# Optimization experiments

Hardware: AMD Instinct MI355X
Metric: run time of the kernel (lower is better)

## Reference

```python
import jax, jax.numpy as jnp
import numpy as np

NA = 100000   # author nodes
NP = 100000   # paper nodes
E = 500000    # edges per relation
H = 128       # hidden size
FA = 256      # author input features
FP = 128      # paper input features
LA = 4        # author labels
LP = 7        # paper labels


def setup_inputs() -> dict:
    key = jax.random.key(0)
    ks = iter(jax.random.split(key, 48))
    def rn(shape, scale=0.05):
        return jax.random.normal(next(ks), shape, jnp.float32) * scale
    inp = {}
    inp['x_author'] = jax.random.normal(next(ks), (NA, FA), jnp.float32)
    inp['x_paper'] = jax.random.normal(next(ks), (NP, FP), jnp.float32)
    inp['edge_index_p2a'] = jax.random.randint(next(ks), (2, E), 0, 100000, jnp.int64)  # row0: paper src, row1: author dst
    inp['edge_index_a2p'] = jax.random.randint(next(ks), (2, E), 0, 100000, jnp.int64)  # row0: author src, row1: paper dst
    # layer 1 convs (per message type): lin_src, lin_dst, lin_update(2H->H)
    inp['w1_p2a_src'] = rn((FP, H)); inp['b1_p2a_src'] = rn((H,))
    inp['w1_p2a_dst'] = rn((FA, H)); inp['b1_p2a_dst'] = rn((H,))
    inp['w1_p2a_upd'] = rn((2 * H, H)); inp['b1_p2a_upd'] = rn((H,))
    inp['w1_a2p_src'] = rn((FA, H)); inp['b1_a2p_src'] = rn((H,))
    inp['w1_a2p_dst'] = rn((FP, H)); inp['b1_a2p_dst'] = rn((H,))
    inp['w1_a2p_upd'] = rn((2 * H, H)); inp['b1_a2p_upd'] = rn((H,))
    # layer 2 convs (all dims = H)
    inp['w2_p2a_src'] = rn((H, H)); inp['b2_p2a_src'] = rn((H,))
    inp['w2_p2a_dst'] = rn((H, H)); inp['b2_p2a_dst'] = rn((H,))
    inp['w2_p2a_upd'] = rn((2 * H, H)); inp['b2_p2a_upd'] = rn((H,))
    inp['w2_a2p_src'] = rn((H, H)); inp['b2_a2p_src'] = rn((H,))
    inp['w2_a2p_dst'] = rn((H, H)); inp['b2_a2p_dst'] = rn((H,))
    inp['w2_a2p_upd'] = rn((2 * H, H)); inp['b2_a2p_upd'] = rn((H,))
    # batchnorm affine params per node type per layer
    inp['g1_a'] = jnp.ones((H,), jnp.float32); inp['be1_a'] = jnp.zeros((H,), jnp.float32)
    inp['g1_p'] = jnp.ones((H,), jnp.float32); inp['be1_p'] = jnp.zeros((H,), jnp.float32)
    inp['g2_a'] = jnp.ones((H,), jnp.float32); inp['be2_a'] = jnp.zeros((H,), jnp.float32)
    inp['g2_p'] = jnp.ones((H,), jnp.float32); inp['be2_p'] = jnp.zeros((H,), jnp.float32)
    # post message-passing heads
    inp['w_post_a'] = rn((H, LA)); inp['b_post_a'] = rn((LA,))
    inp['w_post_p'] = rn((H, LP)); inp['b_post_p'] = rn((LP,))
    return inp


def _mean_agg(x_src, src, dst, n_dst):
    # gather source features along edges, mean-scatter to destination nodes
    msg = x_src[src]                                            # [E, F]
    s = jax.ops.segment_sum(msg, dst, num_segments=n_dst)       # [n_dst, F]
    cnt = jax.ops.segment_sum(jnp.ones((dst.shape[0],), msg.dtype), dst, num_segments=n_dst)
    return s / jnp.maximum(cnt, 1.0)[:, None]


def _conv(x_src, x_dst, src, dst, ws, bs, wd, bd, wu, bu):
    agg = _mean_agg(x_src, src, dst, x_dst.shape[0])
    h = jnp.concatenate([x_dst @ wd + bd, agg @ ws + bs], axis=-1)   # [n_dst, 2H]
    return h @ wu + bu


def _bn_lrelu(x, g, b):
    # BatchNorm1d(eps=1) in training mode (batch stats, biased var) then LeakyReLU(0.01)
    m = x.mean(axis=0)
    v = x.var(axis=0)
    y = g * (x - m) / jnp.sqrt(v + 1.0) + b
    return jnp.where(y >= 0, y, 0.01 * y)


def reference(x_author, x_paper, edge_index_p2a, edge_index_a2p,
              w1_p2a_src, b1_p2a_src, w1_p2a_dst, b1_p2a_dst, w1_p2a_upd, b1_p2a_upd,
              w1_a2p_src, b1_a2p_src, w1_a2p_dst, b1_a2p_dst, w1_a2p_upd, b1_a2p_upd,
              w2_p2a_src, b2_p2a_src, w2_p2a_dst, b2_p2a_dst, w2_p2a_upd, b2_p2a_upd,
              w2_a2p_src, b2_a2p_src, w2_a2p_dst, b2_a2p_dst, w2_a2p_upd, b2_a2p_upd,
              g1_a, be1_a, g1_p, be1_p, g2_a, be2_a, g2_p, be2_p,
              w_post_a, b_post_a, w_post_p, b_post_p):
    src_pa, dst_pa = edge_index_p2a[0], edge_index_p2a[1]
    src_ap, dst_ap = edge_index_a2p[0], edge_index_a2p[1]
    # layer 1: per-message-type conv -> per-node-type BN + LeakyReLU
    h_a = _conv(x_paper, x_author, src_pa, dst_pa, w1_p2a_src, b1_p2a_src, w1_p2a_dst, b1_p2a_dst, w1_p2a_upd, b1_p2a_upd)
    h_p = _conv(x_author, x_paper, src_ap, dst_ap, w1_a2p_src, b1_a2p_src, w1_a2p_dst, b1_a2p_dst, w1_a2p_upd, b1_a2p_upd)
    h_a = _bn_lrelu(h_a, g1_a, be1_a)
    h_p = _bn_lrelu(h_p, g1_p, be1_p)
    # layer 2
    h_a2 = _conv(h_p, h_a, src_pa, dst_pa, w2_p2a_src, b2_p2a_src, w2_p2a_dst, b2_p2a_dst, w2_p2a_upd, b2_p2a_upd)
    h_p2 = _conv(h_a, h_p, src_ap, dst_ap, w2_a2p_src, b2_a2p_src, w2_a2p_dst, b2_a2p_dst, w2_a2p_upd, b2_a2p_upd)
    h_a2 = _bn_lrelu(h_a2, g2_a, be2_a)
    h_p2 = _bn_lrelu(h_p2, g2_p, be2_p)
    # post message-passing heads per node type
    out_a = h_a2 @ w_post_a + b_post_a   # [NA, LA]
    out_p = h_p2 @ w_post_p + b_post_p   # [NP, LP]
    return (out_a, out_p)
```

## Files before the change

### kernel.cpp

```cpp
#include <hip/hip_runtime.h>

#define NN 100000
#define NE 500000
#define HD 128
#define NBLK 391

typedef float f32x4v __attribute__((ext_vector_type(4)));
typedef short s16x8  __attribute__((ext_vector_type(8)));

static __device__ __forceinline__ unsigned f2bf_bits(float f){
  unsigned u = __float_as_uint(f);
  return (u + 0x7FFF + ((u >> 16) & 1)) >> 16;
}

static __device__ __forceinline__ void split8(const float* a, s16x8& hi, s16x8& lo){
  #pragma unroll
  for (int j = 0; j < 8; ++j){
    float f = a[j];
    unsigned hb = f2bf_bits(f);
    float hf = __uint_as_float(hb << 16);
    float lf = f - hf;
    hi[j] = (short)hb;
    lo[j] = (short)f2bf_bits(lf);
  }
}

static __device__ __forceinline__ float4 bn_lrelu4(float4 v, float4 sc, float4 sh){
  v.x = v.x*sc.x + sh.x; v.x = v.x >= 0.f ? v.x : 0.01f*v.x;
  v.y = v.y*sc.y + sh.y; v.y = v.y >= 0.f ? v.y : 0.01f*v.y;
  v.z = v.z*sc.z + sh.z; v.z = v.z >= 0.f ? v.z : 0.01f*v.z;
  v.w = v.w*sc.w + sh.w; v.w = v.w >= 0.f ? v.w : 0.01f*v.w;
  return v;
}

__global__ void k_count(const int* __restrict__ ei_pa, const int* __restrict__ ei_ap,
                        int* __restrict__ deg2){
  int idx = blockIdx.x * 256 + threadIdx.x;
  if (idx < NE)        atomicAdd(&deg2[      ei_pa[NE + idx]], 1);
  else if (idx < 2*NE) atomicAdd(&deg2[NN + ei_ap[NE + (idx - NE)]], 1);
}

__global__ void k_bsum(const int* __restrict__ deg2, int* __restrict__ bsum){
  int rel = blockIdx.x / NBLK, b = blockIdx.x % NBLK;
  int i = b*256 + threadIdx.x;
  int v = (i < NN) ? deg2[rel*NN + i] : 0;
  __shared__ int s[256];
  s[threadIdx.x] = v; __syncthreads();
  for (int o = 128; o > 0; o >>= 1){
    if (threadIdx.x < o) s[threadIdx.x] += s[threadIdx.x + o];
    __syncthreads();
  }
  if (threadIdx.x == 0) bsum[rel*512 + b] = s[0];
}

__global__ void k_bscan(const int* __restrict__ bsum, int* __restrict__ bsoff){
  int rel = blockIdx.x, t = threadIdx.x;
  int v = (t < NBLK) ? bsum[rel*512 + t] : 0;
  __shared__ int s[512];
  s[t] = v; __syncthreads();
  for (int o = 1; o < 512; o <<= 1){
    int x = (t >= o) ? s[t - o] : 0;
    __syncthreads();
    s[t] += x;
    __syncthreads();
  }
  bsoff[rel*512 + t] = s[t] - v;
}

__global__ void k_scanC(const int* __restrict__ deg2, const int* __restrict__ bsoff,
                        int* __restrict__ off2, int* __restrict__ cur2){
  int rel = blockIdx.x / NBLK, b = blockIdx.x % NBLK;
  int i = b*256 + threadIdx.x, t = threadIdx.x;
  int v = (i < NN) ? deg2[rel*NN + i] : 0;
  __shared__ int s[256];
  s[t] = v; __syncthreads();
  for (int o = 1; o < 256; o <<= 1){
    int x = (t >= o) ? s[t - o] : 0;
    __syncthreads();
    s[t] += x;
    __syncthreads();
  }
  if (i < NN){
    int o = bsoff[rel*512 + b] + s[t] - v;
    off2[rel*NN + i] = o;
    cur2[rel*NN + i] = o;
  }
}

__global__ void k_fill(const int* __restrict__ ei_pa, const int* __restrict__ ei_ap,
                       int* __restrict__ cur2,
                       int* __restrict__ col_pa, int* __restrict__ col_ap){
  int idx = blockIdx.x * 256 + threadIdx.x;
  if (idx < NE){
    int s = ei_pa[idx], d = ei_pa[NE + idx];
    int pos = atomicAdd(&cur2[d], 1);
    col_pa[pos] = s;
  } else if (idx < 2*NE){
    int e = idx - NE;
    int s = ei_ap[e], d = ei_ap[NE + e];
    int pos = atomicAdd(&cur2[NN + d], 1);
    col_ap[pos] = s;
  }
}

struct FoldDesc { const float* A; const float* B; short* T; int off; };
struct FoldArgs { FoldDesc d[8]; int rs[9]; };

__global__ void k_fold(FoldArgs fa){
  int row = blockIdx.x;
  int seg = 0;
  #pragma unroll
  for (int s = 0; s < 8; ++s) if (row >= fa.rs[s+1]) seg = s + 1;
  int m = row - fa.rs[seg];
  const float* A = fa.d[seg].A + (size_t)m * 128;
  const float* B = fa.d[seg].B;
  int n = threadIdx.x;
  float acc = 0.f;
  for (int k = 0; k < 128; ++k) acc += A[k] * B[k*128 + n];
  unsigned hb = f2bf_bits(acc);
  float hf = __uint_as_float(hb << 16);
  unsigned lb = f2bf_bits(acc - hf);
  int gkc = fa.d[seg].off + (m >> 5), quad = (m >> 3) & 3, j = m & 7;
  int lane = quad*16 + (n & 15), nt = n >> 4;
  size_t fb = (size_t)((gkc*8 + nt)*2)*512 + lane*8 + j;
  fa.d[seg].T[fb]       = (short)hb;
  fa.d[seg].T[fb + 512] = (short)lb;
}

struct BiasArgs { const float* bd[4]; const float* bs[4]; const float* wu[4];
                  const float* bu[4]; float* outb[4]; };
__global__ void k_biasfold(BiasArgs ba){
  int s = blockIdx.x, j = threadIdx.x;
  const float* wu = ba.wu[s];
  float acc = ba.bu[s][j];
  for (int k = 0; k < 128; ++k)
    acc += ba.bd[s][k] * wu[k*128 + j] + ba.bs[s][k] * wu[(128 + k)*128 + j];
  ba.outb[s][j] = acc;
}

__global__ __launch_bounds__(256)
void k_gemm2(const float* __restrict__ A1, int lda1, int KC1,
             const float* __restrict__ bn1,
             const float* __restrict__ A2, int lda2, int KC2,
             const short* __restrict__ Bf,
             const float* __restrict__ bias, const float* __restrict__ extra,
             float* __restrict__ C, float* __restrict__ stats, int M)
{
  __shared__ __align__(16) char smem[32768];
  short* Bs = (short*)smem;

  const int tid  = threadIdx.x;
  const int wave = tid >> 6, lane = tid & 63;
  const int li   = lane & 15, quad = lane >> 4;
  const int rowT = blockIdx.x * 128 + wave * 32;
  const int KCtot = KC1 + KC2;

  f32x4v acc[2][8];
  #pragma unroll
  for (int mt = 0; mt < 2; ++mt)
    #pragma unroll
    for (int nt = 0; nt < 8; ++nt)
      acc[mt][nt] = (f32x4v){0.f, 0.f, 0.f, 0.f};

  float4 c0[2], c1[2], n0[2], n1[2];
  auto loadA = [&](int gkc, float4* p0, float4* p1){
    const float* Ab; int ld, kk; bool bn;
    if (gkc < KC1){ Ab = A1; ld = lda1; kk = gkc; bn = (bn1 != nullptr); }
    else          { Ab = A2; ld = lda2; kk = gkc - KC1; bn = false; }
    float4 sc0, sc1, sh0, sh1;
    if (bn){
      const float* bsc = bn1 + kk*32 + quad*8;
      sc0 = *(const float4*)bsc;        sc1 = *(const float4*)(bsc + 4);
      sh0 = *(const float4*)(bsc+128);  sh1 = *(const float4*)(bsc + 132);
    }
    #pragma unroll
    for (int mt = 0; mt < 2; ++mt){
      int row = rowT + mt*16 + li;
      if (row < M){
        const float* ap = Ab + (size_t)row*ld + kk*32 + quad*8;
        float4 v0 = *(const float4*)ap;
        float4 v1 = *(const float4*)(ap + 4);
        if (bn){ v0 = bn_lrelu4(v0, sc0, sh0); v1 = bn_lrelu4(v1, sc1, sh1); }
        p0[mt] = v0; p1[mt] = v1;
      } else {
        p0[mt] = make_float4(0.f,0.f,0.f,0.f);
        p1[mt] = make_float4(0.f,0.f,0.f,0.f);
      }
    }
  };
  loadA(0, c0, c1);

  for (int g = 0; g < KCtot; g += 2){
    if (g > 0) __syncthreads();
    const short* src = Bf + (size_t)g*8192;
    #pragma unroll
    for (int c2 = 0; c2 < 8; ++c2){
      int id = c2*256 + tid;
      *(s16x8*)(Bs + id*8) = *(const s16x8*)(src + id*8);
    }
    __syncthreads();
    #pragma unroll
    for (int kc = 0; kc < 2; ++kc){
      int gkc = g + kc;
      if (gkc + 1 < KCtot) loadA(gkc + 1, n0, n1);
      s16x8 ah[2], al[2];
      #pragma unroll
      for (int mt = 0; mt < 2; ++mt){
        float av[8] = {c0[mt].x, c0[mt].y, c0[mt].z, c0[mt].w,
                       c1[mt].x, c1[mt].y, c1[mt].z, c1[mt].w};
        split8(av, ah[mt], al[mt]);
      }
      #pragma unroll
      for (int nt = 0; nt < 8; ++nt){
        const short* bp = Bs + ((kc*8 + nt) << 10) + lane*8;
        s16x8 bh = *(const s16x8*)bp;
        s16x8 bl = *(const s16x8*)(bp + 512);
        #pragma unroll
        for (int mt = 0; mt < 2; ++mt){
          acc[mt][nt] = __builtin_amdgcn_mfma_f32_16x16x32_bf16(ah[mt], bh, acc[mt][nt], 0, 0, 0);
          acc[mt][nt] = __builtin_amdgcn_mfma_f32_16x16x32_bf16(al[mt], bh, acc[mt][nt], 0, 0, 0);
          acc[mt][nt] = __builtin_amdgcn_mfma_f32_16x16x32_bf16(ah[mt], bl, acc[mt][nt], 0, 0, 0);
        }
      }
      #pragma unroll
      for (int mt = 0; mt < 2; ++mt){ c0[mt] = n0[mt]; c1[mt] = n1[mt]; }
    }
  }

  __syncthreads();
  float* Cw = (float*)smem + wave*2048;
  int col4 = lane & 31;
  float4 bias4 = make_float4(0.f,0.f,0.f,0.f);
  if (bias) bias4 = ((const float4*)bias)[col4];
  float4 s1 = make_float4(0.f,0.f,0.f,0.f), s2 = s1;
  #pragma unroll
  for (int mt = 0; mt < 2; ++mt){
    #pragma unroll
    for (int r = 0; r < 4; ++r){
      int lr = quad*4 + r;
      #pragma unroll
      for (int nt = 0; nt < 8; ++nt){
        int c = nt*16 + li;
        int chunk = ((c >> 2) + 2*quad) & 31;
        Cw[lr*128 + chunk*4 + (c & 3)] = acc[mt][nt][r];
      }
    }
    #pragma unroll
    for (int i = 0; i < 8; ++i){
      int lr = i*2 + (lane >> 5);
      int grow = rowT + mt*16 + lr;
      if (grow >= M) continue;
      int chunk = (col4 + 2*(lr >> 2)) & 31;
      float4 v = *(const float4*)(Cw + lr*128 + chunk*4);
      v.x += bias4.x; v.y += bias4.y; v.z += bias4.z; v.w += bias4.w;
      if (extra){
        float4 e = ((const float4*)(extra + (size_t)grow*128))[col4];
        v.x += e.x; v.y += e.y; v.z += e.z; v.w += e.w;
      }
      ((float4*)(C + (size_t)grow*128))[col4] = v;
      s1.x += v.x; s1.y += v.y; s1.z += v.z; s1.w += v.w;
      s2.x += v.x*v.x; s2.y += v.y*v.y; s2.z += v.z*v.z; s2.w += v.w*v.w;
    }
  }
  if (stats){
    __syncthreads();
    float* Ss = (float*)smem;
    ((float4*)Ss)[tid*2]     = s1;
    ((float4*)Ss)[tid*2 + 1] = s2;
    __syncthreads();
    int c = tid & 127, kind = tid >> 7;
    int cc4 = c >> 2, comp = c & 3;
    float s = 0.f;
    #pragma unroll
    for (int wv = 0; wv < 4; ++wv)
      #pragma unroll
      for (int hf = 0; hf < 2; ++hf)
        s += Ss[(wv*64 + hf*32 + cc4)*8 + kind*4 + comp];
    atomicAdd(&stats[kind*128 + c], s);
  }
}

__global__ __launch_bounds__(256)
void k_agg(const float* __restrict__ t, const int* __restrict__ off,
           const int* __restrict__ deg, const int* __restrict__ col,
           float* __restrict__ o, const float* __restrict__ bn){
  int slot = threadIdx.x >> 5, col4 = threadIdx.x & 31;
  int d = blockIdx.x*8 + slot;
  if (d >= NN) return;
  float4 sc4, sh4;
  bool hasbn = (bn != nullptr);
  if (hasbn){ sc4 = ((const float4*)bn)[col4]; sh4 = ((const float4*)(bn+128))[col4]; }
  int s0 = off[d], cnt = deg[d];
  float4 a0 = make_float4(0.f,0.f,0.f,0.f), a1 = a0;
  int i = 0;
  for (; i + 4 <= cnt; i += 4){
    int sa = col[s0+i], sb = col[s0+i+1], sct = col[s0+i+2], sd = col[s0+i+3];
    float4 v0 = ((const float4*)(t + (size_t)sa*128))[col4];
    float4 v1 = ((const float4*)(t + (size_t)sb*128))[col4];
    float4 v2 = ((const float4*)(t + (size_t)sct*128))[col4];
    float4 v3 = ((const float4*)(t + (size_t)sd*128))[col4];
    if (hasbn){
      v0 = bn_lrelu4(v0, sc4, sh4); v1 = bn_lrelu4(v1, sc4, sh4);
      v2 = bn_lrelu4(v2, sc4, sh4); v3 = bn_lrelu4(v3, sc4, sh4);
    }
    a0.x += v0.x + v2.x; a0.y += v0.y + v2.y; a0.z += v0.z + v2.z; a0.w += v0.w + v2.w;
    a1.x += v1.x + v3.x; a1.y += v1.y + v3.y; a1.z += v1.z + v3.z; a1.w += v1.w + v3.w;
  }
  for (; i < cnt; ++i){
    int sa = col[s0+i];
    float4 v0 = ((const float4*)(t + (size_t)sa*128))[col4];
    if (hasbn) v0 = bn_lrelu4(v0, sc4, sh4);
    a0.x += v0.x; a0.y += v0.y; a0.z += v0.z; a0.w += v0.w;
  }
  float inv = 1.0f / (float)(cnt > 0 ? cnt : 1);
  float4 r;
  r.x = (a0.x + a1.x)*inv; r.y = (a0.y + a1.y)*inv;
  r.z = (a0.z + a1.z)*inv; r.w = (a0.w + a1.w)*inv;
  ((float4*)(o + (size_t)d*128))[col4] = r;
}

__global__ void k_bnprep(const float* __restrict__ stats, const float* __restrict__ g,
                         const float* __restrict__ b, float* __restrict__ sc, int M){
  int c = threadIdx.x;
  float invN = 1.0f / (float)M;
  float m  = stats[c] * invN;
  float var = stats[128 + c] * invN - m*m;
  float scale = g[c] / sqrtf(var + 1.0f);
  sc[c] = scale;
  sc[128 + c] = b[c] - m*scale;
}

template<int LC>
__global__ void k_head(const float* __restrict__ h, const float* __restrict__ bn,
                       const float* __restrict__ w, const float* __restrict__ b,
                       float* __restrict__ o, int M){
  __shared__ float ws[128*LC];
  __shared__ float bs[LC];
  __shared__ float bsc[256];
  for (int i = threadIdx.x; i < 128*LC; i += 256) ws[i] = w[i];
  if (threadIdx.x < LC) bs[threadIdx.x] = b[threadIdx.x];
  if (threadIdx.x < 256) bsc[threadIdx.x] = bn[threadIdx.x];
  __syncthreads();
  int r = blockIdx.x*256 + threadIdx.x;
  if (r >= M) return;
  float acc[LC];
  #pragma unroll
  for (int c = 0; c < LC; ++c) acc[c] = bs[c];
  const float4* hr = (const float4*)(h + (size_t)r*128);
  for (int k4 = 0; k4 < 32; ++k4){
    float4 v = hr[k4];
    float4 sc = ((const float4*)bsc)[k4];
    float4 sh = ((const float4*)bsc)[32 + k4];
    v = bn_lrelu4(v, sc, sh);
    int k = k4*4;
    #pragma unroll
    for (int c = 0; c < LC; ++c)
      acc[c] += v.x*ws[k*LC+c] + v.y*ws[(k+1)*LC+c] + v.z*ws[(k+2)*LC+c] + v.w*ws[(k+3)*LC+c];
  }
  #pragma unroll
  for (int c = 0; c < LC; ++c) o[(size_t)r*LC + c] = acc[c];
}

extern "C" void kernel_launch(void* const* d_in, const int* in_sizes, int n_in,
                              void* d_out, int out_size, void* d_ws, size_t ws_size,
                              hipStream_t stream) {
  const float* x_author = (const float*)d_in[0];
  const float* x_paper  = (const float*)d_in[1];
  const int*   ei_pa    = (const int*)d_in[2];
  const int*   ei_ap    = (const int*)d_in[3];

  char* p = (char*)d_ws;
  auto alloc = [&](size_t bytes) -> void* {
    void* r = (void*)p; p += (bytes + 255) & ~(size_t)255; return r;
  };
  short* T_l1a  = (short*)alloc(12u*16384);
  short* T_l1ps = (short*)alloc( 8u*16384);
  short* T_l1pd = (short*)alloc( 4u*16384);
  short* T_l2a  = (short*)alloc( 8u*16384);
  short* T_l2p  = (short*)alloc( 8u*16384);
  float* w1a_b = (float*)alloc(128*4);      float* w1p_b = (float*)alloc(128*4);
  float* w2a_b = (float*)alloc(128*4);      float* w2p_b = (float*)alloc(128*4);
  float* stats4 = (float*)alloc(4*256*4);
  float* bnsc4  = (float*)alloc(4*256*4);
  int* deg2  = (int*)alloc(2*NN*4);
  int* off2  = (int*)alloc(2*NN*4);
  int* cur2  = (int*)alloc(2*NN*4);
  int* col_pa = (int*)alloc(NE*4);
  int* col_ap = (int*)alloc(NE*4);
  int* bsum  = (int*)alloc(1024*4);
  int* bsoff = (int*)alloc(1024*4);
  const size_t NB = (size_t)NN * 128;
  float* B1 = (float*)alloc(NB*4);
  float* B2 = (float*)alloc(NB*4);
  float* B3 = (float*)alloc(NB*4);
  float* B4 = (float*)alloc(NB*4);

  hipMemsetAsync(deg2, 0, 2*NN*4, stream);
  hipMemsetAsync(stats4, 0, 4*256*4, stream);
  k_count<<<(2*NE + 255)/256, 256, 0, stream>>>(ei_pa, ei_ap, deg2);
  k_bsum <<<2*NBLK, 256, 0, stream>>>(deg2, bsum);
  k_bscan<<<2, 512, 0, stream>>>(bsum, bsoff);
  k_scanC<<<2*NBLK, 256, 0, stream>>>(deg2, bsoff, off2, cur2);
  k_fill <<<(2*NE + 255)/256, 256, 0, stream>>>(ei_pa, ei_ap, cur2, col_pa, col_ap);

  FoldArgs fa;
  const float* wu1a = (const float*)d_in[8];
  const float* wu1p = (const float*)d_in[14];
  const float* wu2a = (const float*)d_in[20];
  const float* wu2p = (const float*)d_in[26];
  fa.d[0] = { (const float*)d_in[6],  wu1a,           T_l1a,  0 };
  fa.d[1] = { (const float*)d_in[4],  wu1a + 128*128, T_l1a,  8 };
  fa.d[2] = { (const float*)d_in[10], wu1p + 128*128, T_l1ps, 0 };
  fa.d[3] = { (const float*)d_in[12], wu1p,           T_l1pd, 0 };
  fa.d[4] = { (const float*)d_in[18], wu2a,           T_l2a,  0 };
  fa.d[5] = { (const float*)d_in[16], wu2a + 128*128, T_l2a,  4 };
  fa.d[6] = { (const float*)d_in[24], wu2p,           T_l2p,  0 };
  fa.d[7] = { (const float*)d_in[22], wu2p + 128*128, T_l2p,  4 };
  int rows[8] = {256,128,256,128,128,128,128,128};
  fa.rs[0] = 0;
  for (int i = 0; i < 8; ++i) fa.rs[i+1] = fa.rs[i] + rows[i];
  k_fold<<<fa.rs[8], 128, 0, stream>>>(fa);

  BiasArgs ba;
  ba.bd[0]=(const float*)d_in[7];  ba.bs[0]=(const float*)d_in[5];  ba.wu[0]=wu1a; ba.bu[0]=(const float*)d_in[9];  ba.outb[0]=w1a_b;
  ba.bd[1]=(const float*)d_in[13]; ba.bs[1]=(const float*)d_in[11]; ba.wu[1]=wu1p; ba.bu[1]=(const float*)d_in[15]; ba.outb[1]=w1p_b;
  ba.bd[2]=(const float*)d_in[19]; ba.bs[2]=(const float*)d_in[17]; ba.wu[2]=wu2a; ba.bu[2]=(const float*)d_in[21]; ba.outb[2]=w2a_b;
  ba.bd[3]=(const float*)d_in[25]; ba.bs[3]=(const float*)d_in[23]; ba.wu[3]=wu2p; ba.bu[3]=(const float*)d_in[27]; ba.outb[3]=w2p_b;
  k_biasfold<<<4, 128, 0, stream>>>(ba);

  const int GG = (NN + 127)/128;
  const int AGG_GRID = (NN + 7)/8;
  const int* off_pa = off2;        const int* deg_pa = deg2;
  const int* off_ap = off2 + NN;   const int* deg_ap = deg2 + NN;
  float* st_a1 = stats4;       float* st_p1 = stats4 + 256;
  float* st_a2 = stats4 + 512; float* st_p2 = stats4 + 768;
  float* sc_a1 = bnsc4;        float* sc_p1 = bnsc4 + 256;
  float* sc_a2 = bnsc4 + 512;  float* sc_p2 = bnsc4 + 768;

  k_agg<<<AGG_GRID, 256, 0, stream>>>(x_paper, off_pa, deg_pa, col_pa, B4, nullptr);
  k_gemm2<<<GG, 256, 0, stream>>>(x_author, 256, 8, nullptr, B4, 128, 4, T_l1a,
                                  w1a_b, nullptr, B1, st_a1, NN);
  k_bnprep<<<1, 128, 0, stream>>>(st_a1, (const float*)d_in[28], (const float*)d_in[29], sc_a1, NN);

  k_gemm2<<<GG, 256, 0, stream>>>(x_author, 256, 8, nullptr, nullptr, 0, 0, T_l1ps,
                                  nullptr, nullptr, B3, nullptr, NN);
  k_agg<<<AGG_GRID, 256, 0, stream>>>(B3, off_ap, deg_ap, col_ap, B4, nullptr);
  k_gemm2<<<GG, 256, 0, stream>>>(x_paper, 128, 4, nullptr, nullptr, 0, 0, T_l1pd,
                                  w1p_b, B4, B2, st_p1, NN);
  k_bnprep<<<1, 128, 0, stream>>>(st_p1, (const float*)d_in[30], (const float*)d_in[31], sc_p1, NN);

  k_agg<<<AGG_GRID, 256, 0, stream>>>(B2, off_pa, deg_pa, col_pa, B4, sc_p1);
  k_gemm2<<<GG, 256, 0, stream>>>(B1, 128, 4, sc_a1, B4, 128, 4, T_l2a,
                                  w2a_b, nullptr, B3, st_a2, NN);
  k_bnprep<<<1, 128, 0, stream>>>(st_a2, (const float*)d_in[32], (const float*)d_in[33], sc_a2, NN);
  k_head<4><<<(NN + 255)/256, 256, 0, stream>>>(B3, sc_a2, (const float*)d_in[36],
                                                (const float*)d_in[37], (float*)d_out, NN);

  k_agg<<<AGG_GRID, 256, 0, stream>>>(B1, off_ap, deg_ap, col_ap, B4, sc_a1);
  k_gemm2<<<GG, 256, 0, stream>>>(B2, 128, 4, sc_p1, B4, 128, 4, T_l2p,
                                  w2p_b, nullptr, B3, st_p2, NN);
  k_bnprep<<<1, 128, 0, stream>>>(st_p2, (const float*)d_in[34], (const float*)d_in[35], sc_p2, NN);
  k_head<7><<<(NN + 255)/256, 256, 0, stream>>>(B3, sc_p2, (const float*)d_in[38],
                                                (const float*)d_in[39], (float*)d_out + (size_t)NN*4, NN);
}
```

Baseline: 862.0 us.

## Fuse dual-weight GEMM, gather-in-epilogue, and async LDS double-buffered B staging

```diff
diff --git a/kernel.cpp b/kernel.cpp
--- a/kernel.cpp
+++ b/kernel.cpp
@@ -12,16 +12,18 @@
   unsigned u = __float_as_uint(f);
   return (u + 0x7FFF + ((u >> 16) & 1)) >> 16;
 }
-
-static __device__ __forceinline__ void split8(const float* a, s16x8& hi, s16x8& lo){
-  #pragma unroll
-  for (int j = 0; j < 8; ++j){
-    float f = a[j];
+static __device__ __forceinline__ void split8v(f32x4v v0, f32x4v v1, s16x8& hi, s16x8& lo){
+  #pragma unroll
+  for (int j = 0; j < 4; ++j){
+    float f = v0[j];
     unsigned hb = f2bf_bits(f);
-    float hf = __uint_as_float(hb << 16);
-    float lf = f - hf;
-    hi[j] = (short)hb;
-    lo[j] = (short)f2bf_bits(lf);
+    hi[j] = (short)hb; lo[j] = (short)f2bf_bits(f - __uint_as_float(hb << 16));
+  }
+  #pragma unroll
+  for (int j = 0; j < 4; ++j){
+    float f = v1[j];
+    unsigned hb = f2bf_bits(f);
+    hi[4+j] = (short)hb; lo[4+j] = (short)f2bf_bits(f - __uint_as_float(hb << 16));
   }
 }
 
@@ -30,6 +32,14 @@
   v.y = v.y*sc.y + sh.y; v.y = v.y >= 0.f ? v.y : 0.01f*v.y;
   v.z = v.z*sc.z + sh.z; v.z = v.z >= 0.f ? v.z : 0.01f*v.z;
   v.w = v.w*sc.w + sh.w; v.w = v.w >= 0.f ? v.w : 0.01f*v.w;
+  return v;
+}
+static __device__ __forceinline__ f32x4v bn_lrelu4v(f32x4v v, f32x4v sc, f32x4v sh){
+  #pragma unroll
+  for (int j = 0; j < 4; ++j){
+    float y = v[j]*sc[j] + sh[j];
+    v[j] = y >= 0.f ? y : 0.01f*y;
+  }
   return v;
 }
 
@@ -138,16 +148,22 @@
   ba.outb[s][j] = acc;
 }
 
+template<int DUALB, int GATHER, int BN>
 __global__ __launch_bounds__(256)
-void k_gemm2(const float* __restrict__ A1, int lda1, int KC1,
+void k_gemm3(const float* __restrict__ A1, int lda1, int KC1,
              const float* __restrict__ bn1,
              const float* __restrict__ A2, int lda2, int KC2,
-             const short* __restrict__ Bf,
-             const float* __restrict__ bias, const float* __restrict__ extra,
-             float* __restrict__ C, float* __restrict__ stats, int M)
+             const short* __restrict__ BfA, const short* __restrict__ BfB,
+             const float* __restrict__ bias,
+             const int* __restrict__ goff, const int* __restrict__ gdeg,
+             const int* __restrict__ gcol, const float* __restrict__ gsrc,
+             float* __restrict__ C1, float* __restrict__ C2,
+             float* __restrict__ stats, int M)
 {
-  __shared__ __align__(16) char smem[32768];
-  short* Bs = (short*)smem;
+  constexpr int BUFSZ = DUALB ? 32768 : 16384;
+  constexpr int LDSSZ = 2*BUFSZ + (BN ? 1024 : 0);
+  __shared__ __align__(16) char smem[LDSSZ];
+  float* bnlds = (float*)(smem + 2*BUFSZ);
 
   const int tid  = threadIdx.x;
   const int wave = tid >> 6, lane = tid & 63;
@@ -155,113 +171,182 @@
   const int rowT = blockIdx.x * 128 + wave * 32;
   const int KCtot = KC1 + KC2;
 
-  f32x4v acc[2][8];
+  f32x4v acc1[2][8];
+  f32x4v acc2[2][8];
   #pragma unroll
   for (int mt = 0; mt < 2; ++mt)
     #pragma unroll
-    for (int nt = 0; nt < 8; ++nt)
-      acc[mt][nt] = (f32x4v){0.f, 0.f, 0.f, 0.f};
-
-  float4 c0[2], c1[2], n0[2], n1[2];
-  auto loadA = [&](int gkc, float4* p0, float4* p1){
-    const float* Ab; int ld, kk; bool bn;
-    if (gkc < KC1){ Ab = A1; ld = lda1; kk = gkc; bn = (bn1 != nullptr); }
-    else          { Ab = A2; ld = lda2; kk = gkc - KC1; bn = false; }
-    float4 sc0, sc1, sh0, sh1;
-    if (bn){
-      const float* bsc = bn1 + kk*32 + quad*8;
-      sc0 = *(const float4*)bsc;        sc1 = *(const float4*)(bsc + 4);
-      sh0 = *(const float4*)(bsc+128);  sh1 = *(const float4*)(bsc + 132);
-    }
+    for (int nt = 0; nt < 8; ++nt){
+      acc1[mt][nt] = (f32x4v){0.f, 0.f, 0.f, 0.f};
+      if (DUALB) acc2[mt][nt] = (f32x4v){0.f, 0.f, 0.f, 0.f};
+    }
+
+  const float* b1[2];
+  const float* b2[2];
+  #pragma unroll
+  for (int mt = 0; mt < 2; ++mt){
+    int row = rowT + mt*16 + li;
+    int r = (row < M) ? row : 0;
+    b1[mt] = A1 + (size_t)r*lda1 + quad*8;
+    b2[mt] = A2 ? (A2 + (size_t)r*lda2 + quad*8) : (const float*)nullptr;
+  }
+
+  auto loadA = [&](int gkc, f32x4v (&dst)[2][2]){
     #pragma unroll
     for (int mt = 0; mt < 2; ++mt){
-      int row = rowT + mt*16 + li;
-      if (row < M){
-        const float* ap = Ab + (size_t)row*ld + kk*32 + quad*8;
-        float4 v0 = *(const float4*)ap;
-        float4 v1 = *(const float4*)(ap + 4);
-        if (bn){ v0 = bn_lrelu4(v0, sc0, sh0); v1 = bn_lrelu4(v1, sc1, sh1); }
-        p0[mt] = v0; p1[mt] = v1;
-      } else {
-        p0[mt] = make_float4(0.f,0.f,0.f,0.f);
-        p1[mt] = make_float4(0.f,0.f,0.f,0.f);
+      const float* p = (gkc < KC1) ? (b1[mt] + gkc*32) : (b2[mt] + (gkc - KC1)*32);
+      dst[mt][0] = *(const f32x4v*)p;
+      dst[mt][1] = *(const f32x4v*)(p + 4);
+    }
+  };
+
+  auto stageB = [&](int kc, int bufIdx){
+    char* d = smem + bufIdx * BUFSZ;
+    const char* sA = (const char*)BfA + (size_t)kc * 16384;
+    #pragma unroll
+    for (int c = 0; c < 4; ++c){
+      int off = c*4096 + wave*1024;
+      __builtin_amdgcn_global_load_lds(
+          (const __attribute__((address_space(1))) unsigned int*)(sA + off + lane*16),
+          (__attribute__((address_space(3))) unsigned int*)(d + off),
+          16, 0, 0);
+    }
+    if (DUALB && kc < KC1){
+      const char* sB = (const char*)BfB + (size_t)kc * 16384;
+      #pragma unroll
+      for (int c = 0; c < 4; ++c){
+        int off = c*4096 + wave*1024;
+        __builtin_amdgcn_global_load_lds(
+            (const __attribute__((address_space(1))) unsigned int*)(sB + off + lane*16),
+            (__attribute__((address_space(3))) unsigned int*)(d + 16384 + off),
+            16, 0, 0);
       }
     }
   };
-  loadA(0, c0, c1);
-
-  for (int g = 0; g < KCtot; g += 2){
-    if (g > 0) __syncthreads();
-    const short* src = Bf + (size_t)g*8192;
-    #pragma unroll
-    for (int c2 = 0; c2 < 8; ++c2){
-      int id = c2*256 + tid;
-      *(s16x8*)(Bs + id*8) = *(const s16x8*)(src + id*8);
-    }
-    __syncthreads();
-    #pragma unroll
-    for (int kc = 0; kc < 2; ++kc){
-      int gkc = g + kc;
-      if (gkc + 1 < KCtot) loadA(gkc + 1, n0, n1);
-      s16x8 ah[2], al[2];
+
+  auto computeK = [&](int j, int bufIdx, f32x4v (&a)[2][2]){
+    if (BN && j < KC1){
+      int base = j*32 + quad*8;
+      f32x4v sc0 = *(const f32x4v*)(bnlds + base);
+      f32x4v sc1 = *(const f32x4v*)(bnlds + base + 4);
+      f32x4v sh0 = *(const f32x4v*)(bnlds + base + 128);
+      f32x4v sh1 = *(const f32x4v*)(bnlds + base + 132);
       #pragma unroll
       for (int mt = 0; mt < 2; ++mt){
-        float av[8] = {c0[mt].x, c0[mt].y, c0[mt].z, c0[mt].w,
-                       c1[mt].x, c1[mt].y, c1[mt].z, c1[mt].w};
-        split8(av, ah[mt], al[mt]);
+        a[mt][0] = bn_lrelu4v(a[mt][0], sc0, sh0);
+        a[mt][1] = bn_lrelu4v(a[mt][1], sc1, sh1);
       }
+    }
+    s16x8 ah[2], al[2];
+    #pragma unroll
+    for (int mt = 0; mt < 2; ++mt) split8v(a[mt][0], a[mt][1], ah[mt], al[mt]);
+
+    const short* base = (const short*)(smem + bufIdx*BUFSZ) + lane*8;
+    __builtin_amdgcn_s_setprio(1);
+    #pragma unroll
+    for (int nt = 0; nt < 8; ++nt){
+      const short* bp = base + (nt << 10);
+      s16x8 bh = *(const s16x8*)bp;
+      s16x8 bl = *(const s16x8*)(bp + 512);
+      #pragma unroll
+      for (int mt = 0; mt < 2; ++mt){
+        acc1[mt][nt] = __builtin_amdgcn_mfma_f32_16x16x32_bf16(ah[mt], bh, acc1[mt][nt], 0, 0, 0);
+        acc1[mt][nt] = __builtin_amdgcn_mfma_f32_16x16x32_bf16(al[mt], bh, acc1[mt][nt], 0, 0, 0);
+        acc1[mt][nt] = __builtin_amdgcn_mfma_f32_16x16x32_bf16(ah[mt], bl, acc1[mt][nt], 0, 0, 0);
+      }
+    }
+    if (DUALB && j < KC1){
+      const short* base2 = base + 8192;
       #pragma unroll
       for (int nt = 0; nt < 8; ++nt){
-        const short* bp = Bs + ((kc*8 + nt) << 10) + lane*8;
+        const short* bp = base2 + (nt << 10);
         s16x8 bh = *(const s16x8*)bp;
         s16x8 bl = *(const s16x8*)(bp + 512);
         #pragma unroll
         for (int mt = 0; mt < 2; ++mt){
-          acc[mt][nt] = __builtin_amdgcn_mfma_f32_16x16x32_bf16(ah[mt], bh, acc[mt][nt], 0, 0, 0);
-          acc[mt][nt] = __builtin_amdgcn_mfma_f32_16x16x32_bf16(al[mt], bh, acc[mt][nt], 0, 0, 0);
-          acc[mt][nt] = __builtin_amdgcn_mfma_f32_16x16x32_bf16(ah[mt], bl, acc[mt][nt], 0, 0, 0);
+          acc2[mt][nt] = __builtin_amdgcn_mfma_f32_16x16x32_bf16(ah[mt], bh, acc2[mt][nt], 0, 0, 0);
+          acc2[mt][nt] = __builtin_amdgcn_mfma_f32_16x16x32_bf16(al[mt], bh, acc2[mt][nt], 0, 0, 0);
+          acc2[mt][nt] = __builtin_amdgcn_mfma_f32_16x16x32_bf16(ah[mt], bl, acc2[mt][nt], 0, 0, 0);
         }
       }
-      #pragma unroll
-      for (int mt = 0; mt < 2; ++mt){ c0[mt] = n0[mt]; c1[mt] = n1[mt]; }
+    }
+    __builtin_amdgcn_s_setprio(0);
+  };
+
+  if (BN) bnlds[tid] = bn1[tid];
+  f32x4v aC[2][2], aN1[2][2], aN2[2][2];
+  stageB(0, 0);
+  loadA(0, aC);
+  loadA(1, aN1);
+  if (BN) asm volatile("s_waitcnt lgkmcnt(0)" ::: "memory");
+
+  for (int j = 0; j < KCtot; ++j){
+    if (j + 1 < KCtot) asm volatile("s_waitcnt vmcnt(4)" ::: "memory");
+    else               asm volatile("s_waitcnt vmcnt(0)" ::: "memory");
+    __builtin_amdgcn_s_barrier();
+    __builtin_amdgcn_sched_barrier(0);
+    if (j + 1 < KCtot) stageB(j + 1, (j + 1) & 1);
+    if (j + 2 < KCtot) loadA(j + 2, aN2);
+    computeK(j, j & 1, aC);
+    #pragma unroll
+    for (int mt = 0; mt < 2; ++mt){
+      aC[mt][0] = aN1[mt][0]; aC[mt][1] = aN1[mt][1];
+      aN1[mt][0] = aN2[mt][0]; aN1[mt][1] = aN2[mt][1];
     }
   }
 
   __syncthreads();
   float* Cw = (float*)smem + wave*2048;
   int col4 = lane & 31;
-  float4 bias4 = make_float4(0.f,0.f,0.f,0.f);
-  if (bias) bias4 = ((const float4*)bias)[col4];
   float4 s1 = make_float4(0.f,0.f,0.f,0.f), s2 = s1;
-  #pragma unroll
-  for (int mt = 0; mt < 2; ++mt){
-    #pragma unroll
-    for (int r = 0; r < 4; ++r){
-      int lr = quad*4 + r;
-      #pragma unroll
-      for (int nt = 0; nt < 8; ++nt){
-        int c = nt*16 + li;
-        int chunk = ((c >> 2) + 2*quad) & 31;
-        Cw[lr*128 + chunk*4 + (c & 3)] = acc[mt][nt][r];
+
+  auto epi_pass = [&](f32x4v (&ac)[2][8], float* Cout, const float* bptr,
+                      bool wStats){
+    float4 bias4 = make_float4(0.f,0.f,0.f,0.f);
+    if (bptr) bias4 = ((const float4*)bptr)[col4];
+    #pragma unroll
+    for (int mt = 0; mt < 2; ++mt){
+      #pragma unroll
+      for (int r = 0; r < 4; ++r){
+        int lr = quad*4 + r;
+        #pragma unroll
+        for (int nt = 0; nt < 8; ++nt){
+          int c = nt*16 + li;
+          int chunk = ((c >> 2) + 2*quad) & 31;
+          Cw[lr*128 + chunk*4 + (c & 3)] = ac[mt][nt][r];
+        }
       }
-    }
-    #pragma unroll
-    for (int i = 0; i < 8; ++i){
-      int lr = i*2 + (lane >> 5);
-      int grow = rowT + mt*16 + lr;
-      if (grow >= M) continue;
-      int chunk = (col4 + 2*(lr >> 2)) & 31;
-      float4 v = *(const float4*)(Cw + lr*128 + chunk*4);
-      v.x += bias4.x; v.y += bias4.y; v.z += bias4.z; v.w += bias4.w;
-      if (extra){
-        float4 e = ((const float4*)(extra + (size_t)grow*128))[col4];
-        v.x += e.x; v.y += e.y; v.z += e.z; v.w += e.w;
+      #pragma unroll
+      for (int i = 0; i < 8; ++i){
+        int lr = i*2 + (lane >> 5);
+        int grow = rowT + mt*16 + lr;
+        if (grow >= M) continue;
+        int chunk = (col4 + 2*(lr >> 2)) & 31;
+        float4 v = *(const float4*)(Cw + lr*128 + chunk*4);
+        v.x += bias4.x; v.y += bias4.y; v.z += bias4.z; v.w += bias4.w;
+        if (GATHER && wStats){
+          int cnt = gdeg[grow], s0g = goff[grow];
+          float4 g = make_float4(0.f,0.f,0.f,0.f);
+          for (int e = 0; e < cnt; ++e){
+            int src = gcol[s0g + e];
+            float4 gv = ((const float4*)(gsrc + ((size_t)src << 7)))[col4];
+            g.x += gv.x; g.y += gv.y; g.z += gv.z; g.w += gv.w;
+          }
+          float inv = 1.0f / (float)(cnt > 0 ? cnt : 1);
+          v.x += g.x*inv; v.y += g.y*inv; v.z += g.z*inv; v.w += g.w*inv;
+        }
+        ((float4*)(Cout + ((size_t)grow << 7)))[col4] = v;
+        if (wStats){
+          s1.x += v.x; s1.y += v.y; s1.z += v.z; s1.w += v.w;
+          s2.x += v.x*v.x; s2.y += v.y*v.y; s2.z += v.z*v.z; s2.w += v.w*v.w;
+        }
       }
-      ((float4*)(C + (size_t)grow*128))[col4] = v;
-      s1.x += v.x; s1.y += v.y; s1.z += v.z; s1.w += v.w;
-      s2.x += v.x*v.x; s2.y += v.y*v.y; s2.z += v.z*v.z; s2.w += v.w*v.w;
-    }
-  }
+    }
+  };
+
+  epi_pass(acc1, C1, bias, stats != nullptr);
+  if (DUALB) epi_pass(acc2, C2, nullptr, false);
+
   if (stats){
     __syncthreads();
     float* Ss = (float*)smem;
@@ -295,10 +380,10 @@
   int i = 0;
   for (; i + 4 <= cnt; i += 4){
     int sa = col[s0+i], sb = col[s0+i+1], sct = col[s0+i+2], sd = col[s0+i+3];
-    float4 v0 = ((const float4*)(t + (size_t)sa*128))[col4];
-    float4 v1 = ((const float4*)(t + (size_t)sb*128))[col4];
-    float4 v2 = ((const float4*)(t + (size_t)sct*128))[col4];
-    float4 v3 = ((const float4*)(t + (size_t)sd*128))[col4];
+    float4 v0 = ((const float4*)(t + ((size_t)sa << 7)))[col4];
+    float4 v1 = ((const float4*)(t + ((size_t)sb << 7)))[col4];
+    float4 v2 = ((const float4*)(t + ((size_t)sct << 7)))[col4];
+    float4 v3 = ((const float4*)(t + ((size_t)sd << 7)))[col4];
     if (hasbn){
       v0 = bn_lrelu4(v0, sc4, sh4); v1 = bn_lrelu4(v1, sc4, sh4);
       v2 = bn_lrelu4(v2, sc4, sh4); v3 = bn_lrelu4(v3, sc4, sh4);
@@ -308,7 +393,7 @@
   }
   for (; i < cnt; ++i){
     int sa = col[s0+i];
-    float4 v0 = ((const float4*)(t + (size_t)sa*128))[col4];
+    float4 v0 = ((const float4*)(t + ((size_t)sa << 7)))[col4];
     if (hasbn) v0 = bn_lrelu4(v0, sc4, sh4);
     a0.x += v0.x; a0.y += v0.y; a0.z += v0.z; a0.w += v0.w;
   }
@@ -316,7 +401,7 @@
   float4 r;
   r.x = (a0.x + a1.x)*inv; r.y = (a0.y + a1.y)*inv;
   r.z = (a0.z + a1.z)*inv; r.w = (a0.w + a1.w)*inv;
-  ((float4*)(o + (size_t)d*128))[col4] = r;
+  ((float4*)(o + ((size_t)d << 7)))[col4] = r;
 }
 
 __global__ void k_bnprep(const float* __restrict__ stats, const float* __restrict__ g,
@@ -346,7 +431,7 @@
   float acc[LC];
   #pragma unroll
   for (int c = 0; c < LC; ++c) acc[c] = bs[c];
-  const float4* hr = (const float4*)(h + (size_t)r*128);
+  const float4* hr = (const float4*)(h + ((size_t)r << 7));
   for (int k4 = 0; k4 < 32; ++k4){
     float4 v = hr[k4];
     float4 sc = ((const float4*)bsc)[k4];
@@ -438,28 +523,29 @@
   float* sc_a2 = bnsc4 + 512;  float* sc_p2 = bnsc4 + 768;
 
   k_agg<<<AGG_GRID, 256, 0, stream>>>(x_paper, off_pa, deg_pa, col_pa, B4, nullptr);
-  k_gemm2<<<GG, 256, 0, stream>>>(x_author, 256, 8, nullptr, B4, 128, 4, T_l1a,
-                                  w1a_b, nullptr, B1, st_a1, NN);
+  k_gemm3<1,0,0><<<GG, 256, 0, stream>>>(
+      x_author, 256, 8, nullptr, B4, 128, 4, T_l1a, T_l1ps, w1a_b,
+      nullptr, nullptr, nullptr, nullptr, B1, B3, st_a1, NN);
   k_bnprep<<<1, 128, 0, stream>>>(st_a1, (const float*)d_in[28], (const float*)d_in[29], sc_a1, NN);
 
-  k_gemm2<<<GG, 256, 0, stream>>>(x_author, 256, 8, nullptr, nullptr, 0, 0, T_l1ps,
-                                  nullptr, nullptr, B3, nullptr, NN);
-  k_agg<<<AGG_GRID, 256, 0, stream>>>(B3, off_ap, deg_ap, col_ap, B4, nullptr);
-  k_gemm2<<<GG, 256, 0, stream>>>(x_paper, 128, 4, nullptr, nullptr, 0, 0, T_l1pd,
-                                  w1p_b, B4, B2, st_p1, NN);
+  k_gemm3<0,1,0><<<GG, 256, 0, stream>>>(
+      x_paper, 128, 4, nullptr, nullptr, 128, 0, T_l1pd, nullptr, w1p_b,
+      off_ap, deg_ap, col_ap, B3, B2, nullptr, st_p1, NN);
   k_bnprep<<<1, 128, 0, stream>>>(st_p1, (const float*)d_in[30], (const float*)d_in[31], sc_p1, NN);
 
   k_agg<<<AGG_GRID, 256, 0, stream>>>(B2, off_pa, deg_pa, col_pa, B4, sc_p1);
-  k_gemm2<<<GG, 256, 0, stream>>>(B1, 128, 4, sc_a1, B4, 128, 4, T_l2a,
-                                  w2a_b, nullptr, B3, st_a2, NN);
+  k_gemm3<0,0,1><<<GG, 256, 0, stream>>>(
+      B1, 128, 4, sc_a1, B4, 128, 4, T_l2a, nullptr, w2a_b,
+      nullptr, nullptr, nullptr, nullptr, B3, nullptr, st_a2, NN);
   k_bnprep<<<1, 128, 0, stream>>>(st_a2, (const float*)d_in[32], (const float*)d_in[33], sc_a2, NN);
   k_head<4><<<(NN + 255)/256, 256, 0, stream>>>(B3, sc_a2, (const float*)d_in[36],
                                                 (const float*)d_in[37], (float*)d_out, NN);
 
   k_agg<<<AGG_GRID, 256, 0, stream>>>(B1, off_ap, deg_ap, col_ap, B4, sc_a1);
-  k_gemm2<<<GG, 256, 0, stream>>>(B2, 128, 4, sc_p1, B4, 128, 4, T_l2p,
-                                  w2p_b, nullptr, B3, st_p2, NN);
+  k_gemm3<0,0,1><<<GG, 256, 0, stream>>>(
+      B2, 128, 4, sc_p1, B4, 128, 4, T_l2p, nullptr, w2p_b,
+      nullptr, nullptr, nullptr, nullptr, B1, nullptr, st_p2, NN);
   k_bnprep<<<1, 128, 0, stream>>>(st_p2, (const float*)d_in[34], (const float*)d_in[35], sc_p2, NN);
-  k_head<7><<<(NN + 255)/256, 256, 0, stream>>>(B3, sc_p2, (const float*)d_in[38],
+  k_head<7><<<(NN + 255)/256, 256, 0, stream>>>(B1, sc_p2, (const float*)d_in[38],
                                                 (const float*)d_in[39], (float*)d_out + (size_t)NN*4, NN);
 }
```

Result: slower. 944.6 us (+9.6%).
